# Kernel optimization log

Measured on AMD Instinct MI355X. Metric: run time of the kernel, lower is better.

Reference implementation:

```python
import jax, jax.numpy as jnp
import numpy as np

ALPHA = 0.2     # LeakyReLU negative slope
NEG = -1e9      # mask value for non-edges (matches -1000000000)
N, S, O, H, E = 8192, 128, 64, 4, 262144


def setup_inputs() -> dict:
    key = jax.random.key(0)
    ks = jax.random.split(key, 6)
    x = jax.random.normal(ks[0], (1, N, S), jnp.float32)
    edges = jax.random.randint(ks[1], (2, E), 0, N, dtype=jnp.int64)
    values = jnp.ones((E,), jnp.float32)
    # xavier_normal with gain=1.414
    W_heads = jax.random.normal(ks[2], (H, S, O), jnp.float32) * (1.414 * np.sqrt(2.0 / (S + O)))
    a_heads = jax.random.normal(ks[3], (H, 2 * O), jnp.float32) * (1.414 * np.sqrt(2.0 / (1 + 2 * O)))
    lin_w = jax.random.normal(ks[4], (1, H), jnp.float32) * 0.5
    lin_b = jnp.zeros((1,), jnp.float32)
    return {"x": x, "edges": edges, "values": values, "W_heads": W_heads,
            "a_heads": a_heads, "lin_w": lin_w, "lin_b": lin_b}


def reference(x, edges, values, W_heads, a_heads, lin_w, lin_b):
    b, n, s = x.shape
    Ntot = b * n
    xf = x.reshape(Ntot, s)
    # per-head projection: [H, N, O]
    h = jnp.einsum('ns,hso->hno', xf, W_heads)
    e0, e1 = edges[0], edges[1]
    Od = h.shape[-1]
    # per-edge attention logits for all heads: a . [h_src || h_dst], shape [H, E]
    atts = (jnp.einsum('heo,ho->he', h[:, e0, :], a_heads[:, :Od])
            + jnp.einsum('heo,ho->he', h[:, e1, :], a_heads[:, Od:]))
    atts = jax.nn.leaky_relu(atts, negative_slope=ALPHA)
    # combine heads with a 1-output linear: [E]
    mt = (atts.T @ lin_w.T + lin_b)[:, 0]
    new_values = values * mt
    # scatter to dense NxN (duplicate edges sum, like sparse coo to_dense)
    dense = jnp.zeros((Ntot, Ntot), x.dtype).at[e0, e1].add(new_values)
    a_dense = jnp.zeros((Ntot, Ntot), values.dtype).at[e0, e1].add(values)
    mask = jnp.where(a_dense == 0, NEG, jnp.where(a_dense == 1, 0.0, a_dense))
    # softmax over dim 0, as in the original
    return jax.nn.softmax(dense + mask, axis=0)
```

## Files before the change

kernel.cpp:

```cpp
#include <hip/hip_runtime.h>
#include <math.h>


#define ALPHA 0.2f
constexpr int S = 128;
constexpr int O = 64;
constexpr int H = 4;
constexpr int CAP = 128;

__global__ void __launch_bounds__(256) k1_zero_scores(
    const float* __restrict__ x, const float* __restrict__ W, const float* __restrict__ a,
    float4* __restrict__ s_src4, float4* __restrict__ s_dst4,
    int* __restrict__ col_cursor, float4* __restrict__ out4,
    int N, size_t n4tot)
{
    __shared__ float wsbuf[2 * H * S];
    int tid = threadIdx.x;
    int gt = blockIdx.x * 256 + tid;

    if (blockIdx.x * 256 < N) {
        for (int t = tid; t < 2 * H * S; t += 256) {
            int which = t / (H * S);
            int hs = t % (H * S);
            int h = hs / S, s = hs % S;
            const float* Wr = W + ((size_t)h * S + s) * O;
            const float* av = a + h * 2 * O + which * O;
            float acc = 0.f;
            for (int o = 0; o < O; ++o) acc += Wr[o] * av[o];
            wsbuf[t] = acc;
        }
        __syncthreads();
        int n = gt;
        if (n < N) {
            col_cursor[n] = 0;
            const float* wsrc = wsbuf;
            const float* wdst = wsbuf + H * S;
            const float4* xr = (const float4*)(x + (size_t)n * S);
            float accs[H] = {0, 0, 0, 0}, accd[H] = {0, 0, 0, 0};
            for (int i = 0; i < S / 4; ++i) {
                float4 v = xr[i];
#pragma unroll
                for (int h = 0; h < H; ++h) {
                    const float* p = wsrc + h * S + i * 4;
                    const float* q = wdst + h * S + i * 4;
                    accs[h] += v.x * p[0] + v.y * p[1] + v.z * p[2] + v.w * p[3];
                    accd[h] += v.x * q[0] + v.y * q[1] + v.z * q[2] + v.w * q[3];
                }
            }
            s_src4[n] = make_float4(accs[0], accs[1], accs[2], accs[3]);
            s_dst4[n] = make_float4(accd[0], accd[1], accd[2], accd[3]);
        }
    }

    const float4 z4 = make_float4(0.f, 0.f, 0.f, 0.f);
    size_t GT = (size_t)gridDim.x * 256;
    for (size_t k = gt; k < n4tot; k += GT) out4[k] = z4;
}

__global__ void __launch_bounds__(256) k2_scatter(
    const int* __restrict__ edges, const float* __restrict__ values,
    const float4* __restrict__ s_src4, const float4* __restrict__ s_dst4,
    const float* __restrict__ lin_w, const float* __restrict__ lin_b,
    int* __restrict__ col_cursor, int4* __restrict__ col_ent, int N, int E)
{
    int e = blockIdx.x * 256 + threadIdx.x;
    if (e >= E) return;
    int r = edges[e];
    int c = edges[(size_t)E + e];
    if ((unsigned)r >= (unsigned)N || (unsigned)c >= (unsigned)N) return;
    float4 ss = s_src4[r];
    float4 sd = s_dst4[c];
    float att0 = ss.x + sd.x, att1 = ss.y + sd.y, att2 = ss.z + sd.z, att3 = ss.w + sd.w;
    att0 = att0 >= 0.f ? att0 : ALPHA * att0;
    att1 = att1 >= 0.f ? att1 : ALPHA * att1;
    att2 = att2 >= 0.f ? att2 : ALPHA * att2;
    att3 = att3 >= 0.f ? att3 : ALPHA * att3;
    float mt = lin_b[0] + att0 * lin_w[0] + att1 * lin_w[1] + att2 * lin_w[2] + att3 * lin_w[3];
    float av = values[e];
    float nv = av * mt;
    int posc = atomicAdd(&col_cursor[c], 1);
    if (posc < CAP) {
        int4 ent;
        ent.x = r;
        ent.y = __float_as_int(nv);
        ent.z = __float_as_int(av);
        ent.w = 0;
        col_ent[(size_t)c * CAP + posc] = ent;
    }
}

__global__ void __launch_bounds__(256) k3_softmax(
    const int4* __restrict__ col_ent, const int* __restrict__ col_cursor,
    float* __restrict__ out, int N)
{
    int wave = threadIdx.x >> 6, lane = threadIdx.x & 63;
    int j = blockIdx.x * 4 + wave;
    if (j >= N) return;
    int m = col_cursor[j];
    if (m > CAP) m = CAP;
    if (m == 0) {
        float u = 1.0f / (float)N;
        for (int i = lane; i < N; i += 64) out[(size_t)i * N + j] = u;
        return;
    }
    const int4* base = col_ent + (size_t)j * CAP;
    if (m <= 64) {
        bool mine = lane < m;
        int r; float v, av;
        if (mine) {
            int4 ent = base[lane];
            r = ent.x; v = __int_as_float(ent.y); av = __int_as_float(ent.z);
        } else {
            r = -1 - lane; v = 0.f; av = 0.f;
        }
        float dsum = 0.f, asum = 0.f;
        bool first = true;
        for (int l = 0; l < 64; ++l) {
            int rl = __shfl(r, l);
            float vl = __shfl(v, l);
            float al = __shfl(av, l);
            if (rl == r) {
                dsum += vl; asum += al;
                if (l < lane) first = false;
            }
        }
        float mask = (asum == 1.0f) ? 0.f : asum;
        float val = dsum + mask;
        float lmax = (mine && first) ? val : -INFINITY;
#pragma unroll
        for (int off = 32; off; off >>= 1) lmax = fmaxf(lmax, __shfl_xor(lmax, off));
        float ex = (mine && first) ? expf(val - lmax) : 0.f;
        float lsum = ex;
#pragma unroll
        for (int off = 32; off; off >>= 1) lsum += __shfl_xor(lsum, off);
        float inv = 1.0f / lsum;
        if (mine) out[(size_t)r * N + j] = expf(val - lmax) * inv;
    } else {
        float lmax = -INFINITY;
        for (int k = lane; k < m; k += 64) {
            int rk = base[k].x;
            bool first = true;
            float ds = 0.f, as = 0.f;
            for (int l = 0; l < m; ++l) {
                int4 el = base[l];
                if (el.x == rk) {
                    if (l < k) first = false;
                    ds += __int_as_float(el.y);
                    as += __int_as_float(el.z);
                }
            }
            if (first) {
                float mk = (as == 1.0f) ? 0.f : as;
                lmax = fmaxf(lmax, ds + mk);
            }
        }
#pragma unroll
        for (int off = 32; off; off >>= 1) lmax = fmaxf(lmax, __shfl_xor(lmax, off));
        float lsum = 0.f;
        for (int k = lane; k < m; k += 64) {
            int rk = base[k].x;
            bool first = true;
            float ds = 0.f, as = 0.f;
            for (int l = 0; l < m; ++l) {
                int4 el = base[l];
                if (el.x == rk) {
                    if (l < k) first = false;
                    ds += __int_as_float(el.y);
                    as += __int_as_float(el.z);
                }
            }
            if (first) {
                float mk = (as == 1.0f) ? 0.f : as;
                lsum += expf(ds + mk - lmax);
            }
        }
#pragma unroll
        for (int off = 32; off; off >>= 1) lsum += __shfl_xor(lsum, off);
        float inv = 1.0f / lsum;
        for (int k = lane; k < m; k += 64) {
            int rk = base[k].x;
            float ds = 0.f, as = 0.f;
            for (int l = 0; l < m; ++l) {
                int4 el = base[l];
                if (el.x == rk) {
                    ds += __int_as_float(el.y);
                    as += __int_as_float(el.z);
                }
            }
            float mk = (as == 1.0f) ? 0.f : as;
            out[(size_t)rk * N + j] = expf(ds + mk - lmax) * inv;
        }
    }
}

extern "C" void kernel_launch(void* const* d_in, const int* in_sizes, int n_in,
                              void* d_out, int out_size, void* d_ws, size_t ws_size,
                              hipStream_t stream) {
    const float* x = (const float*)d_in[0];
    const int* edges = (const int*)d_in[1];
    const float* values = (const float*)d_in[2];
    const float* W = (const float*)d_in[3];
    const float* a = (const float*)d_in[4];
    const float* lin_w = (const float*)d_in[5];
    const float* lin_b = (const float*)d_in[6];
    float* out = (float*)d_out;

    int N = in_sizes[0] / S;
    int E = in_sizes[2];

    char* wsb = (char*)d_ws;
    size_t off = 0;
    auto alloc = [&](size_t bytes) -> void* {
        void* p = wsb + off;
        off += (bytes + 255) & ~(size_t)255;
        return p;
    };
    float4* s_src4 = (float4*)alloc((size_t)N * 16);
    float4* s_dst4 = (float4*)alloc((size_t)N * 16);
    int* col_cursor = (int*)alloc((size_t)N * 4);
    int4* col_ent = (int4*)alloc((size_t)N * CAP * 16);

    size_t n4tot = (size_t)N * N / 4;
    k1_zero_scores<<<2048, 256, 0, stream>>>(x, W, a, s_src4, s_dst4,
                                             col_cursor, (float4*)out, N, n4tot);
    k2_scatter<<<(E + 255) / 256, 256, 0, stream>>>(edges, values, s_src4, s_dst4,
                                                    lin_w, lin_b, col_cursor, col_ent, N, E);
    k3_softmax<<<(N + 3) / 4, 256, 0, stream>>>(col_ent, col_cursor, out, N);
}
```

Before: 102.7 us.

## Fuse per-edge score computation and scatter into the output-zeroing kernel

Merges the node-score and edge-scatter kernels into the zeroing kernel. 1024 blocks handle edges while 2048 separate blocks clear the dense output concurrently, and the cursor reset moves to a memset. Each edge now recomputes its source and destination projections from the two full 128-float x rows instead of reading precomputed per-node scores. This removes one launch and the intermediate score buffers but multiplies the x reads and FLOPs per edge by about 32x. The softmax shuffle loop is also trimmed to iterate only m lanes.

New measurement: 144.6 us. +40.8%, slower.

```diff
diff --git a/kernel.cpp b/kernel.cpp
--- a/kernel.cpp
+++ b/kernel.cpp
@@ -7,18 +7,19 @@
 constexpr int O = 64;
 constexpr int H = 4;
 constexpr int CAP = 128;
-
-__global__ void __launch_bounds__(256) k1_zero_scores(
+constexpr int SCAT_BLOCKS = 1024;
+constexpr int ZERO_BLOCKS = 2048;
+
+__global__ void __launch_bounds__(256) k1_zero_scatter(
     const float* __restrict__ x, const float* __restrict__ W, const float* __restrict__ a,
-    float4* __restrict__ s_src4, float4* __restrict__ s_dst4,
-    int* __restrict__ col_cursor, float4* __restrict__ out4,
-    int N, size_t n4tot)
+    const int* __restrict__ edges, const float* __restrict__ values,
+    const float* __restrict__ lin_w, const float* __restrict__ lin_b,
+    int* __restrict__ cursor, int4* __restrict__ col_ent,
+    float4* __restrict__ out4, int N, int E, size_t n4tot)
 {
-    __shared__ float wsbuf[2 * H * S];
     int tid = threadIdx.x;
-    int gt = blockIdx.x * 256 + tid;
-
-    if (blockIdx.x * 256 < N) {
+    if (blockIdx.x < (unsigned)SCAT_BLOCKS) {
+        __shared__ float wsbuf[2 * H * S];
         for (int t = tid; t < 2 * H * S; t += 256) {
             int which = t / (H * S);
             int hs = t % (H * S);
@@ -30,66 +31,56 @@
             wsbuf[t] = acc;
         }
         __syncthreads();
-        int n = gt;
-        if (n < N) {
-            col_cursor[n] = 0;
-            const float* wsrc = wsbuf;
-            const float* wdst = wsbuf + H * S;
-            const float4* xr = (const float4*)(x + (size_t)n * S);
-            float accs[H] = {0, 0, 0, 0}, accd[H] = {0, 0, 0, 0};
-            for (int i = 0; i < S / 4; ++i) {
-                float4 v = xr[i];
+        int e = blockIdx.x * 256 + tid;
+        if (e < E) {
+            int r = edges[e];
+            int c = edges[(size_t)E + e];
+            if ((unsigned)r < (unsigned)N && (unsigned)c < (unsigned)N) {
+                const float* wsrc = wsbuf;
+                const float* wdst = wsbuf + H * S;
+                const float4* xr = (const float4*)(x + (size_t)r * S);
+                const float4* xc = (const float4*)(x + (size_t)c * S);
+                float accs[H] = {0, 0, 0, 0}, accd[H] = {0, 0, 0, 0};
+                for (int i = 0; i < S / 4; ++i) {
+                    float4 vr = xr[i];
+                    float4 vc = xc[i];
+#pragma unroll
+                    for (int h = 0; h < H; ++h) {
+                        const float* p = wsrc + h * S + i * 4;
+                        const float* q = wdst + h * S + i * 4;
+                        accs[h] += vr.x * p[0] + vr.y * p[1] + vr.z * p[2] + vr.w * p[3];
+                        accd[h] += vc.x * q[0] + vc.y * q[1] + vc.z * q[2] + vc.w * q[3];
+                    }
+                }
+                float mt = lin_b[0];
 #pragma unroll
                 for (int h = 0; h < H; ++h) {
-                    const float* p = wsrc + h * S + i * 4;
-                    const float* q = wdst + h * S + i * 4;
-                    accs[h] += v.x * p[0] + v.y * p[1] + v.z * p[2] + v.w * p[3];
-                    accd[h] += v.x * q[0] + v.y * q[1] + v.z * q[2] + v.w * q[3];
-                }
-            }
-            s_src4[n] = make_float4(accs[0], accs[1], accs[2], accs[3]);
-            s_dst4[n] = make_float4(accd[0], accd[1], accd[2], accd[3]);
-        }
-    }
-
-    const float4 z4 = make_float4(0.f, 0.f, 0.f, 0.f);
-    size_t GT = (size_t)gridDim.x * 256;
-    for (size_t k = gt; k < n4tot; k += GT) out4[k] = z4;
-}
-
-__global__ void __launch_bounds__(256) k2_scatter(
-    const int* __restrict__ edges, const float* __restrict__ values,
-    const float4* __restrict__ s_src4, const float4* __restrict__ s_dst4,
-    const float* __restrict__ lin_w, const float* __restrict__ lin_b,
-    int* __restrict__ col_cursor, int4* __restrict__ col_ent, int N, int E)
-{
-    int e = blockIdx.x * 256 + threadIdx.x;
-    if (e >= E) return;
-    int r = edges[e];
-    int c = edges[(size_t)E + e];
-    if ((unsigned)r >= (unsigned)N || (unsigned)c >= (unsigned)N) return;
-    float4 ss = s_src4[r];
-    float4 sd = s_dst4[c];
-    float att0 = ss.x + sd.x, att1 = ss.y + sd.y, att2 = ss.z + sd.z, att3 = ss.w + sd.w;
-    att0 = att0 >= 0.f ? att0 : ALPHA * att0;
-    att1 = att1 >= 0.f ? att1 : ALPHA * att1;
-    att2 = att2 >= 0.f ? att2 : ALPHA * att2;
-    att3 = att3 >= 0.f ? att3 : ALPHA * att3;
-    float mt = lin_b[0] + att0 * lin_w[0] + att1 * lin_w[1] + att2 * lin_w[2] + att3 * lin_w[3];
-    float av = values[e];
-    float nv = av * mt;
-    int posc = atomicAdd(&col_cursor[c], 1);
-    if (posc < CAP) {
-        int4 ent;
-        ent.x = r;
-        ent.y = __float_as_int(nv);
-        ent.z = __float_as_int(av);
-        ent.w = 0;
-        col_ent[(size_t)c * CAP + posc] = ent;
+                    float att = accs[h] + accd[h];
+                    att = att >= 0.f ? att : ALPHA * att;
+                    mt += att * lin_w[h];
+                }
+                float av = values[e];
+                float nv = av * mt;
+                int pos = atomicAdd(&cursor[c], 1);
+                if (pos < CAP) {
+                    int4 ent;
+                    ent.x = r;
+                    ent.y = __float_as_int(nv);
+                    ent.z = __float_as_int(av);
+                    ent.w = 0;
+                    col_ent[(size_t)c * CAP + pos] = ent;
+                }
+            }
+        }
+    } else {
+        const float4 z4 = make_float4(0.f, 0.f, 0.f, 0.f);
+        size_t gt = (size_t)(blockIdx.x - SCAT_BLOCKS) * 256 + tid;
+        size_t GT = (size_t)(gridDim.x - SCAT_BLOCKS) * 256;
+        for (size_t k = gt; k < n4tot; k += GT) out4[k] = z4;
     }
 }
 
-__global__ void __launch_bounds__(256) k3_softmax(
+__global__ void __launch_bounds__(256) k2_softmax(
     const int4* __restrict__ col_ent, const int* __restrict__ col_cursor,
     float* __restrict__ out, int N)
 {
@@ -115,7 +106,7 @@
         }
         float dsum = 0.f, asum = 0.f;
         bool first = true;
-        for (int l = 0; l < 64; ++l) {
+        for (int l = 0; l < m; ++l) {
             int rl = __shfl(r, l);
             float vl = __shfl(v, l);
             float al = __shfl(av, l);
@@ -215,15 +206,13 @@
         off += (bytes + 255) & ~(size_t)255;
         return p;
     };
-    float4* s_src4 = (float4*)alloc((size_t)N * 16);
-    float4* s_dst4 = (float4*)alloc((size_t)N * 16);
-    int* col_cursor = (int*)alloc((size_t)N * 4);
+    int* cursor = (int*)alloc((size_t)N * 4);
     int4* col_ent = (int4*)alloc((size_t)N * CAP * 16);
 
     size_t n4tot = (size_t)N * N / 4;
-    k1_zero_scores<<<2048, 256, 0, stream>>>(x, W, a, s_src4, s_dst4,
-                                             col_cursor, (float4*)out, N, n4tot);
-    k2_scatter<<<(E + 255) / 256, 256, 0, stream>>>(edges, values, s_src4, s_dst4,
-                                                    lin_w, lin_b, col_cursor, col_ent, N, E);
-    k3_softmax<<<(N + 3) / 4, 256, 0, stream>>>(col_ent, col_cursor, out, N);
+    hipMemsetAsync(cursor, 0, (size_t)N * sizeof(int), stream);
+    k1_zero_scatter<<<SCAT_BLOCKS + ZERO_BLOCKS, 256, 0, stream>>>(
+        x, W, a, edges, values, lin_w, lin_b, cursor, col_ent,
+        (float4*)out, N, E, n4tot);
+    k2_softmax<<<(N + 3) / 4, 256, 0, stream>>>(col_ent, cursor, out, N);
 }
```
